# Performance work log

Hardware: AMD Instinct MI355X
Metric: run time of the kernel (lower is better)

The kernel has to match this reference:

```python
import jax, jax.numpy as jnp
import numpy as np

N = 50000
E = 800000
IN_C = 128
HID = 32
HEADS = 8
OUT_C = 64
NEG_SLOPE = 0.2


def setup_inputs() -> dict:
    key = jax.random.key(0)
    ks = jax.random.split(key, 12)
    x = jax.random.normal(ks[0], (N, IN_C), dtype=jnp.float32)
    edge_index = jax.random.randint(ks[1], (2, E), 0, N, dtype=jnp.int64)
    s = 0.05
    W1 = jax.random.normal(ks[2], (IN_C, HEADS * HID), dtype=jnp.float32) * s
    a1_src = jax.random.normal(ks[3], (HEADS, HID), dtype=jnp.float32) * s
    a1_dst = jax.random.normal(ks[4], (HEADS, HID), dtype=jnp.float32) * s
    b1 = jnp.zeros((HEADS * HID,), dtype=jnp.float32)
    W2 = jax.random.normal(ks[5], (HEADS * HID, OUT_C), dtype=jnp.float32) * s
    a2_src = jax.random.normal(ks[6], (1, OUT_C), dtype=jnp.float32) * s
    a2_dst = jax.random.normal(ks[7], (1, OUT_C), dtype=jnp.float32) * s
    b2 = jnp.zeros((OUT_C,), dtype=jnp.float32)
    return {"x": x, "edge_index": edge_index, "W1": W1, "a1_src": a1_src,
            "a1_dst": a1_dst, "b1": b1, "W2": W2, "a2_src": a2_src,
            "a2_dst": a2_dst, "b2": b2}


def gat_conv(x, W, a_src, a_dst, bias, src, dst, concat):
    # x: [N, F_in]; W: [F_in, H*C]; a_src/a_dst: [H, C]
    H, C = a_src.shape
    h = (x @ W).reshape(N, H, C)                      # [N, H, C]
    alpha_s = jnp.einsum('nhc,hc->nh', h, a_src)      # [N, H]
    alpha_d = jnp.einsum('nhc,hc->nh', h, a_dst)
    e = alpha_s[src] + alpha_d[dst]                   # [E, H]
    e = jnp.where(e >= 0, e, NEG_SLOPE * e)           # leaky relu
    # segment softmax over destination nodes
    m = jax.ops.segment_max(e, dst, num_segments=N)   # [N, H]
    e = jnp.exp(e - m[dst])
    z = jax.ops.segment_sum(e, dst, num_segments=N)   # [N, H]
    alpha = e / z[dst]                                # [E, H]
    msg = h[src] * alpha[:, :, None]                  # [E, H, C]
    out = jax.ops.segment_sum(msg, dst, num_segments=N)  # [N, H, C]
    if concat:
        out = out.reshape(N, H * C)
    else:
        out = out.mean(axis=1)
    return out + bias


def reference(x, edge_index, W1, a1_src, a1_dst, b1, W2, a2_src, a2_dst, b2):
    src, dst = edge_index[0], edge_index[1]
    # dropout omitted (eval mode)
    h = gat_conv(x, W1, a1_src, a1_dst, b1, src, dst, concat=True)
    h = jax.nn.elu(h)
    out = gat_conv(h, W2, a2_src, a2_dst, b2, src, dst, concat=False)
    return out
```

## Files before the change

### kernel.cpp

```cpp
#include <hip/hip_runtime.h>
#include <cstdint>
#include <cstddef>

#define N_NODES 50000
#define N_EDGES 800000
#define INC 128
#define HID 32
#define HEADS 8
#define OUTC 64
#define F1 (HEADS * HID)
#define NEG 0.2f
#define CAP 64

typedef unsigned short bf16_t;
typedef __attribute__((ext_vector_type(8))) short bf16x8;
typedef __attribute__((ext_vector_type(4))) float f32x4;

__device__ __forceinline__ float bf2f(bf16_t u) {
  union { unsigned int i; float f; } v;
  v.i = ((unsigned int)u) << 16;
  return v.f;
}
__device__ __forceinline__ bf16_t f2bf(float x) {
  union { float f; unsigned int u; } v;
  v.f = x;
  unsigned int r = v.u + 0x7FFFu + ((v.u >> 16) & 1u);
  return (bf16_t)(r >> 16);
}
__device__ __forceinline__ float lrexp(float v) {
  return expf((v >= 0.f) ? v : NEG * v);
}

template <bool AF32, int HPT, int HTOT>
__global__ __launch_bounds__(256) void mfma_gemm_fused(
    const void* __restrict__ Av, const float* __restrict__ Wf,
    bf16_t* __restrict__ C, const float* __restrict__ a_src,
    const float* __restrict__ a_dst, float* __restrict__ as,
    float* __restrict__ ad, int M, int N, int K,
    const int* __restrict__ srcE, const int* __restrict__ dstE,
    int* __restrict__ cnt, int* __restrict__ bucket) {
  constexpr int BM = 64, BN = 64, BK = 64;
  __shared__ union SM {
    struct { bf16_t A[BM * BK]; bf16_t B[BN * BK]; } st;
    struct { float ct[64][65]; float pr[64][4]; } epi;
  } sm;

  const int tid = threadIdx.x;

  if (cnt != nullptr) {
    int eid = (blockIdx.y * gridDim.x + blockIdx.x) * 256 + tid;
    if (eid < N_EDGES) {
      int dd = dstE[eid];
      int pos = atomicAdd(&cnt[dd], 1);
      bucket[(size_t)dd * CAP + pos] = srcE[eid];
    }
  }

  const int wave = tid >> 6, lane = tid & 63;
  const int wm = (wave >> 1) * 32, wn = (wave & 1) * 32;
  const int lr = lane & 15, lq = lane >> 4;
  const int m0 = blockIdx.y * BM, n0 = blockIdx.x * BN;
  const float* A32 = (const float*)Av;
  const bf16_t* A16 = (const bf16_t*)Av;

  f32x4 acc[2][2] = {};

  for (int k0 = 0; k0 < K; k0 += BK) {
#pragma unroll
    for (int p = 0; p < 2; p++) {
      int id = p * 256 + tid;
      int r = id >> 3, c = id & 7;
      int gm = m0 + r;
      uint4 v = make_uint4(0, 0, 0, 0);
      if constexpr (AF32) {
        if (gm < M) {
          const float4* ap =
              reinterpret_cast<const float4*>(&A32[(size_t)gm * K + k0 + c * 8]);
          float4 v0 = ap[0], v1 = ap[1];
          union { bf16_t h[8]; uint4 u; } pk;
          pk.h[0] = f2bf(v0.x); pk.h[1] = f2bf(v0.y);
          pk.h[2] = f2bf(v0.z); pk.h[3] = f2bf(v0.w);
          pk.h[4] = f2bf(v1.x); pk.h[5] = f2bf(v1.y);
          pk.h[6] = f2bf(v1.z); pk.h[7] = f2bf(v1.w);
          v = pk.u;
        }
      } else {
        if (gm < M) v = *reinterpret_cast<const uint4*>(&A16[(size_t)gm * K + k0 + c * 8]);
      }
      *reinterpret_cast<uint4*>(&sm.st.A[r * BK + ((c ^ (r & 7)) * 8)]) = v;
    }
#pragma unroll
    for (int p = 0; p < 2; p++) {
      int id = p * 256 + tid;
      int r = id >> 3, c = id & 7;
      union { bf16_t h[8]; uint4 u; } pk;
#pragma unroll
      for (int j = 0; j < 8; j++)
        pk.h[j] = f2bf(Wf[(size_t)(k0 + c * 8 + j) * N + n0 + r]);
      *reinterpret_cast<uint4*>(&sm.st.B[r * BK + ((c ^ (r & 7)) * 8)]) = pk.u;
    }
    __syncthreads();
#pragma unroll
    for (int kk = 0; kk < 2; kk++) {
      bf16x8 af[2], bfr[2];
#pragma unroll
      for (int mi = 0; mi < 2; mi++) {
        int rr = wm + mi * 16 + lr;
        af[mi] = *reinterpret_cast<const bf16x8*>(
            &sm.st.A[rr * BK + (((kk * 4 + lq) ^ (rr & 7)) * 8)]);
      }
#pragma unroll
      for (int ni = 0; ni < 2; ni++) {
        int rr = wn + ni * 16 + lr;
        bfr[ni] = *reinterpret_cast<const bf16x8*>(
            &sm.st.B[rr * BK + (((kk * 4 + lq) ^ (rr & 7)) * 8)]);
      }
#pragma unroll
      for (int mi = 0; mi < 2; mi++)
#pragma unroll
        for (int ni = 0; ni < 2; ni++)
          acc[mi][ni] = __builtin_amdgcn_mfma_f32_16x16x32_bf16(
              af[mi], bfr[ni], acc[mi][ni], 0, 0, 0);
    }
    __syncthreads();
  }

#pragma unroll
  for (int mi = 0; mi < 2; mi++)
#pragma unroll
    for (int ni = 0; ni < 2; ni++)
#pragma unroll
      for (int r = 0; r < 4; r++)
        sm.epi.ct[wm + mi * 16 + lq * 4 + r][wn + ni * 16 + lr] = acc[mi][ni][r];
  __syncthreads();

#pragma unroll
  for (int mi = 0; mi < 2; mi++)
#pragma unroll
    for (int ni = 0; ni < 2; ni++)
#pragma unroll
      for (int r = 0; r < 4; r++) {
        int gm = m0 + wm + mi * 16 + lq * 4 + r;
        if (gm < M)
          C[(size_t)gm * N + n0 + wn + ni * 16 + lr] = f2bf(acc[mi][ni][r]);
      }

  {
    int row = tid >> 2, part = tid & 3;
    int gn = m0 + row;
    const float* av = ((part & 2) ? a_dst : a_src) + n0 + (part & 1) * 32;
    float dot = 0.f;
#pragma unroll
    for (int c = 0; c < 32; c++) dot += sm.epi.ct[row][(part & 1) * 32 + c] * av[c];
    if constexpr (HPT == 2) {
      if (gn < M) {
        float* tgt = (part & 2) ? ad : as;
        tgt[(size_t)gn * HTOT + (n0 >> 5) + (part & 1)] = dot;
      }
    } else {
      sm.epi.pr[row][part] = dot;
      __syncthreads();
      if (part == 0 && gn < M) {
        as[gn] = sm.epi.pr[row][0] + sm.epi.pr[row][1];
        ad[gn] = sm.epi.pr[row][2] + sm.epi.pr[row][3];
      }
    }
  }
}

__global__ __launch_bounds__(256) void gat_aggr1(
    const int* __restrict__ cnt, const int* __restrict__ bucket,
    const float* __restrict__ as, const float* __restrict__ ad,
    const bf16_t* __restrict__ hb, const float* __restrict__ bias,
    bf16_t* __restrict__ outp) {
  int d = blockIdx.x * 4 + (threadIdx.x >> 6);
  int lane = threadIdx.x & 63;
  if (d >= N_NODES) return;
  int deg = cnt[d];
  const int* bkt = bucket + (size_t)d * CAP;
  const int sh = lane & 7;
  const int es = lane >> 3;
  const int ah = lane >> 3;
  float ad_h = ad[(size_t)d * 8 + sh];
  float a0 = 0.f, a1 = 0.f, a2 = 0.f, a3 = 0.f, zacc = 0.f;

  if (deg > 0) {
    int ei = es;
    int s_reg = bkt[(ei < deg) ? ei : deg - 1];
    float w_reg = (ei < deg) ? lrexp(as[(size_t)s_reg * 8 + sh] + ad_h) : 0.f;

    for (int cb = 0; cb < deg; cb += 8) {
      const bf16_t* bs[8];
#pragma unroll
      for (int e = 0; e < 8; e++)
        bs[e] = hb + (size_t)__builtin_amdgcn_readlane(s_reg, e << 3) * F1;
      uint2 g[8];
#pragma unroll
      for (int e = 0; e < 8; e++)
        g[e] = *reinterpret_cast<const uint2*>(bs[e] + 4 * lane);
      float w_cur = w_reg;
      zacc += w_reg;
      int nxt = cb + 8;
      if (nxt < deg) {
        int ei2 = nxt + es;
        s_reg = bkt[(ei2 < deg) ? ei2 : deg - 1];
        w_reg = (ei2 < deg) ? lrexp(as[(size_t)s_reg * 8 + sh] + ad_h) : 0.f;
      }
#pragma unroll
      for (int e = 0; e < 8; e++) {
        float wv = __shfl(w_cur, (e << 3) | ah);
        union { uint2 u; bf16_t h[4]; } ld;
        ld.u = g[e];
        a0 += bf2f(ld.h[0]) * wv;
        a1 += bf2f(ld.h[1]) * wv;
        a2 += bf2f(ld.h[2]) * wv;
        a3 += bf2f(ld.h[3]) * wv;
      }
    }
  }

  float zr = zacc;
  zr += __shfl_xor(zr, 8);
  zr += __shfl_xor(zr, 16);
  zr += __shfl_xor(zr, 32);
  float z = __shfl(zr, ah);

  float inv = (deg > 0) ? (1.f / z) : 0.f;
  float4 bv = *reinterpret_cast<const float4*>(&bias[4 * lane]);
  float v0 = a0 * inv + bv.x;
  float v1 = a1 * inv + bv.y;
  float v2 = a2 * inv + bv.z;
  float v3 = a3 * inv + bv.w;
  v0 = (v0 > 0.f) ? v0 : expm1f(v0);
  v1 = (v1 > 0.f) ? v1 : expm1f(v1);
  v2 = (v2 > 0.f) ? v2 : expm1f(v2);
  v3 = (v3 > 0.f) ? v3 : expm1f(v3);
  union { bf16_t h[4]; uint2 u; } pk;
  pk.h[0] = f2bf(v0); pk.h[1] = f2bf(v1); pk.h[2] = f2bf(v2); pk.h[3] = f2bf(v3);
  *reinterpret_cast<uint2*>(&outp[(size_t)d * F1 + 4 * lane]) = pk.u;
}

__global__ __launch_bounds__(256) void gat_aggr2(
    const int* __restrict__ cnt, const int* __restrict__ bucket,
    const float* __restrict__ as, const float* __restrict__ ad,
    const bf16_t* __restrict__ hb, const float* __restrict__ bias,
    float* __restrict__ outp) {
  int d = blockIdx.x * 32 + (threadIdx.x >> 3);
  int sub = threadIdx.x & 7;
  if (d >= N_NODES) return;
  int deg = cnt[d];
  const int* bkt = bucket + (size_t)d * CAP;
  float ad_d = ad[d];
  float acc[8] = {};
  float zacc = 0.f;

  if (deg > 0) {
    int ei = sub;
    int s_reg = bkt[(ei < deg) ? ei : deg - 1];
    float w_reg = (ei < deg) ? lrexp(as[s_reg] + ad_d) : 0.f;

    for (int cb = 0; cb < deg; cb += 8) {
      int sv[8];
#pragma unroll
      for (int e = 0; e < 8; e++) sv[e] = __shfl(s_reg, e, 8);
      uint4 g[8];
#pragma unroll
      for (int e = 0; e < 8; e++)
        g[e] = *reinterpret_cast<const uint4*>(&hb[(size_t)sv[e] * OUTC + 8 * sub]);
      float w_cur = w_reg;
      zacc += w_reg;
      int nxt = cb + 8;
      if (nxt < deg) {
        int ei2 = nxt + sub;
        s_reg = bkt[(ei2 < deg) ? ei2 : deg - 1];
        w_reg = (ei2 < deg) ? lrexp(as[s_reg] + ad_d) : 0.f;
      }
#pragma unroll
      for (int e = 0; e < 8; e++) {
        float wv = __shfl(w_cur, e, 8);
        union { uint4 u; bf16_t h[8]; } ld;
        ld.u = g[e];
#pragma unroll
        for (int q = 0; q < 8; q++) acc[q] += bf2f(ld.h[q]) * wv;
      }
    }
  }

  float zr = zacc;
  zr += __shfl_xor(zr, 1, 8);
  zr += __shfl_xor(zr, 2, 8);
  zr += __shfl_xor(zr, 4, 8);

  float inv = (deg > 0) ? (1.f / zr) : 0.f;
  float4 o0, o1;
  o0.x = acc[0] * inv + bias[8 * sub + 0];
  o0.y = acc[1] * inv + bias[8 * sub + 1];
  o0.z = acc[2] * inv + bias[8 * sub + 2];
  o0.w = acc[3] * inv + bias[8 * sub + 3];
  o1.x = acc[4] * inv + bias[8 * sub + 4];
  o1.y = acc[5] * inv + bias[8 * sub + 5];
  o1.z = acc[6] * inv + bias[8 * sub + 6];
  o1.w = acc[7] * inv + bias[8 * sub + 7];
  *reinterpret_cast<float4*>(&outp[(size_t)d * OUTC + 8 * sub]) = o0;
  *reinterpret_cast<float4*>(&outp[(size_t)d * OUTC + 8 * sub + 4]) = o1;
}

extern "C" void kernel_launch(void* const* d_in, const int* in_sizes, int n_in,
                              void* d_out, int out_size, void* d_ws, size_t ws_size,
                              hipStream_t stream) {
  const float* x      = (const float*)d_in[0];
  const int*   ei     = (const int*)d_in[1];
  const float* W1     = (const float*)d_in[2];
  const float* a1_src = (const float*)d_in[3];
  const float* a1_dst = (const float*)d_in[4];
  const float* b1     = (const float*)d_in[5];
  const float* W2     = (const float*)d_in[6];
  const float* a2_src = (const float*)d_in[7];
  const float* a2_dst = (const float*)d_in[8];
  const float* b2     = (const float*)d_in[9];

  const int* src = ei;
  const int* dst = ei + N_EDGES;
  float* out = (float*)d_out;

  char* base = (char*)d_ws;
  size_t off = 0;
  auto carve = [&](size_t bytes) {
    void* q = base + off;
    off += (bytes + 255) & ~size_t(255);
    return q;
  };
  bf16_t* h1b  = (bf16_t*)carve((size_t)N_NODES * F1 * 2);
  bf16_t* o1b  = (bf16_t*)carve((size_t)N_NODES * F1 * 2);
  bf16_t* h2b  = (bf16_t*)carve((size_t)N_NODES * OUTC * 2);
  float* as1 = (float*)carve((size_t)N_NODES * HEADS * 4);
  float* ad1 = (float*)carve((size_t)N_NODES * HEADS * 4);
  float* as2 = (float*)carve((size_t)N_NODES * 4);
  float* ad2 = (float*)carve((size_t)N_NODES * 4);
  int* cnt = (int*)carve((size_t)N_NODES * 4);
  int* bucket = (int*)carve((size_t)N_NODES * CAP * 4);

  hipMemsetAsync(cnt, 0, N_NODES * sizeof(int), stream);

  mfma_gemm_fused<true, 2, HEADS><<<dim3(F1 / 64, (N_NODES + 63) / 64), 256, 0, stream>>>(
      x, W1, h1b, a1_src, a1_dst, as1, ad1, N_NODES, F1, INC, src, dst, cnt, bucket);

  gat_aggr1<<<(N_NODES + 3) / 4, 256, 0, stream>>>(cnt, bucket, as1, ad1, h1b, b1, o1b);

  mfma_gemm_fused<false, 1, 1><<<dim3(OUTC / 64, (N_NODES + 63) / 64), 256, 0, stream>>>(
      o1b, W2, h2b, a2_src, a2_dst, as2, ad2, N_NODES, OUTC, F1,
      nullptr, nullptr, nullptr, nullptr);

  gat_aggr2<<<(N_NODES + 31) / 32, 256, 0, stream>>>(cnt, bucket, as2, ad2, h2b, b2, out);
}
```

Before: 260.8 us.

## Pre-transpose weights to bf16 and load B fragments directly from global

Adds a prep kernel that zeroes the edge counters (replacing the memset) and writes transposed bf16 copies of W1 and W2. The GEMM then loads B fragments straight from global memory into registers in MFMA layout, skipping the shared-memory B stage. It also replaces the per-block strided fp32-to-bf16 conversion of W. The output epilogue now writes C as packed 16-byte rows from the shared tile instead of scattered 2-byte stores. This adds a small kernel launch, and the B loads are no longer staged through LDS, so more global/L2 traffic is issued per wave.

```diff
diff --git a/kernel.cpp b/kernel.cpp
--- a/kernel.cpp
+++ b/kernel.cpp
@@ -31,9 +31,24 @@
   return expf((v >= 0.f) ? v : NEG * v);
 }
 
+__global__ __launch_bounds__(256) void prep(
+    const float* __restrict__ W1, const float* __restrict__ W2,
+    bf16_t* __restrict__ W1T, bf16_t* __restrict__ W2T, int* __restrict__ cnt) {
+  int t = blockIdx.x * 256 + threadIdx.x;
+  if (t < N_NODES) cnt[t] = 0;
+  if (t < INC * F1) {
+    int k = t >> 8, n = t & 255;
+    W1T[(size_t)n * INC + k] = f2bf(W1[t]);
+  }
+  if (t < F1 * OUTC) {
+    int k = t >> 6, n = t & 63;
+    W2T[(size_t)n * F1 + k] = f2bf(W2[t]);
+  }
+}
+
 template <bool AF32, int HPT, int HTOT>
 __global__ __launch_bounds__(256) void mfma_gemm_fused(
-    const void* __restrict__ Av, const float* __restrict__ Wf,
+    const void* __restrict__ Av, const bf16_t* __restrict__ Wt,
     bf16_t* __restrict__ C, const float* __restrict__ a_src,
     const float* __restrict__ a_dst, float* __restrict__ as,
     float* __restrict__ ad, int M, int N, int K,
@@ -41,7 +56,7 @@
     int* __restrict__ cnt, int* __restrict__ bucket) {
   constexpr int BM = 64, BN = 64, BK = 64;
   __shared__ union SM {
-    struct { bf16_t A[BM * BK]; bf16_t B[BN * BK]; } st;
+    bf16_t A[BM * BK];
     struct { float ct[64][65]; float pr[64][4]; } epi;
   } sm;
 
@@ -66,6 +81,16 @@
   f32x4 acc[2][2] = {};
 
   for (int k0 = 0; k0 < K; k0 += BK) {
+    bf16x8 bcur[2][2];
+#pragma unroll
+    for (int ni = 0; ni < 2; ni++) {
+      const size_t brow = (size_t)(n0 + wn + ni * 16 + lr) * K;
+#pragma unroll
+      for (int kk = 0; kk < 2; kk++)
+        bcur[kk][ni] = *reinterpret_cast<const bf16x8*>(
+            &Wt[brow + k0 + kk * 32 + lq * 8]);
+    }
+
 #pragma unroll
     for (int p = 0; p < 2; p++) {
       int id = p * 256 + tid;
@@ -87,40 +112,24 @@
       } else {
         if (gm < M) v = *reinterpret_cast<const uint4*>(&A16[(size_t)gm * K + k0 + c * 8]);
       }
-      *reinterpret_cast<uint4*>(&sm.st.A[r * BK + ((c ^ (r & 7)) * 8)]) = v;
-    }
-#pragma unroll
-    for (int p = 0; p < 2; p++) {
-      int id = p * 256 + tid;
-      int r = id >> 3, c = id & 7;
-      union { bf16_t h[8]; uint4 u; } pk;
-#pragma unroll
-      for (int j = 0; j < 8; j++)
-        pk.h[j] = f2bf(Wf[(size_t)(k0 + c * 8 + j) * N + n0 + r]);
-      *reinterpret_cast<uint4*>(&sm.st.B[r * BK + ((c ^ (r & 7)) * 8)]) = pk.u;
+      *reinterpret_cast<uint4*>(&sm.A[r * BK + ((c ^ (r & 7)) * 8)]) = v;
     }
     __syncthreads();
 #pragma unroll
     for (int kk = 0; kk < 2; kk++) {
-      bf16x8 af[2], bfr[2];
+      bf16x8 af[2];
 #pragma unroll
       for (int mi = 0; mi < 2; mi++) {
         int rr = wm + mi * 16 + lr;
         af[mi] = *reinterpret_cast<const bf16x8*>(
-            &sm.st.A[rr * BK + (((kk * 4 + lq) ^ (rr & 7)) * 8)]);
-      }
-#pragma unroll
-      for (int ni = 0; ni < 2; ni++) {
-        int rr = wn + ni * 16 + lr;
-        bfr[ni] = *reinterpret_cast<const bf16x8*>(
-            &sm.st.B[rr * BK + (((kk * 4 + lq) ^ (rr & 7)) * 8)]);
+            &sm.A[rr * BK + (((kk * 4 + lq) ^ (rr & 7)) * 8)]);
       }
 #pragma unroll
       for (int mi = 0; mi < 2; mi++)
 #pragma unroll
         for (int ni = 0; ni < 2; ni++)
           acc[mi][ni] = __builtin_amdgcn_mfma_f32_16x16x32_bf16(
-              af[mi], bfr[ni], acc[mi][ni], 0, 0, 0);
+              af[mi], bcur[kk][ni], acc[mi][ni], 0, 0, 0);
     }
     __syncthreads();
   }
@@ -134,16 +143,19 @@
         sm.epi.ct[wm + mi * 16 + lq * 4 + r][wn + ni * 16 + lr] = acc[mi][ni][r];
   __syncthreads();
 
-#pragma unroll
-  for (int mi = 0; mi < 2; mi++)
-#pragma unroll
-    for (int ni = 0; ni < 2; ni++)
-#pragma unroll
-      for (int r = 0; r < 4; r++) {
-        int gm = m0 + wm + mi * 16 + lq * 4 + r;
-        if (gm < M)
-          C[(size_t)gm * N + n0 + wn + ni * 16 + lr] = f2bf(acc[mi][ni][r]);
-      }
+  {
+    int row = tid >> 2, ch = tid & 3;
+    int gm = m0 + row;
+    if (gm < M) {
+      union { bf16_t h[8]; uint4 u; } pk0, pk1;
+#pragma unroll
+      for (int c = 0; c < 8; c++) pk0.h[c] = f2bf(sm.epi.ct[row][ch * 16 + c]);
+#pragma unroll
+      for (int c = 0; c < 8; c++) pk1.h[c] = f2bf(sm.epi.ct[row][ch * 16 + 8 + c]);
+      *reinterpret_cast<uint4*>(&C[(size_t)gm * N + n0 + ch * 16]) = pk0.u;
+      *reinterpret_cast<uint4*>(&C[(size_t)gm * N + n0 + ch * 16 + 8]) = pk1.u;
+    }
+  }
 
   {
     int row = tid >> 2, part = tid & 3;
@@ -339,16 +351,18 @@
   float* ad2 = (float*)carve((size_t)N_NODES * 4);
   int* cnt = (int*)carve((size_t)N_NODES * 4);
   int* bucket = (int*)carve((size_t)N_NODES * CAP * 4);
-
-  hipMemsetAsync(cnt, 0, N_NODES * sizeof(int), stream);
+  bf16_t* w1t = (bf16_t*)carve((size_t)F1 * INC * 2);
+  bf16_t* w2t = (bf16_t*)carve((size_t)OUTC * F1 * 2);
+
+  prep<<<(N_NODES + 255) / 256, 256, 0, stream>>>(W1, W2, w1t, w2t, cnt);
 
   mfma_gemm_fused<true, 2, HEADS><<<dim3(F1 / 64, (N_NODES + 63) / 64), 256, 0, stream>>>(
-      x, W1, h1b, a1_src, a1_dst, as1, ad1, N_NODES, F1, INC, src, dst, cnt, bucket);
+      x, w1t, h1b, a1_src, a1_dst, as1, ad1, N_NODES, F1, INC, src, dst, cnt, bucket);
 
   gat_aggr1<<<(N_NODES + 3) / 4, 256, 0, stream>>>(cnt, bucket, as1, ad1, h1b, b1, o1b);
 
   mfma_gemm_fused<false, 1, 1><<<dim3(OUTC / 64, (N_NODES + 63) / 64), 256, 0, stream>>>(
-      o1b, W2, h2b, a2_src, a2_dst, as2, ad2, N_NODES, OUTC, F1,
+      o1b, w2t, h2b, a2_src, a2_dst, as2, ad2, N_NODES, OUTC, F1,
       nullptr, nullptr, nullptr, nullptr);
 
   gat_aggr2<<<(N_NODES + 31) / 32, 256, 0, stream>>>(cnt, bucket, as2, ad2, h2b, b2, out);
```

New measurement: 242.3 us. -7.1%, faster.
